# Kernel tuning notes

Measured on AMD Instinct MI355X. Metric: run time of the kernel, lower is better.

## Reference

```python
import jax, jax.numpy as jnp
import numpy as np

B, K, D = 2, 2048, 1024
H, DQ, DV = 16, 64, 64
DFF = 4096
ATT_SIZE = 256
LN_EPS = 1e-5


def _layernorm(x, g, b):
    mu = jnp.mean(x, axis=-1, keepdims=True)
    var = jnp.mean(jnp.square(x - mu), axis=-1, keepdims=True)
    return (x - mu) * jax.lax.rsqrt(var + LN_EPS) * g + b


def setup_inputs() -> dict:
    key = jax.random.key(0)
    ks = jax.random.split(key, 16)
    s = lambda d: 1.0 / np.sqrt(d)
    return {
        "x": jax.random.normal(ks[0], (B, K, D), dtype=jnp.float32),
        "Wq": jax.random.normal(ks[1], (D, H * DQ), dtype=jnp.float32) * s(D),
        "bq": jnp.zeros((H * DQ,), dtype=jnp.float32),
        "Wk": jax.random.normal(ks[2], (D, H * DQ), dtype=jnp.float32) * s(D),
        "bk": jnp.zeros((H * DQ,), dtype=jnp.float32),
        "Wv": jax.random.normal(ks[3], (D, H * DV), dtype=jnp.float32) * s(D),
        "bv": jnp.zeros((H * DV,), dtype=jnp.float32),
        "Wo": jax.random.normal(ks[4], (H * DV, D), dtype=jnp.float32) * s(H * DV),
        "bo": jnp.zeros((D,), dtype=jnp.float32),
        "W1": jax.random.normal(ks[5], (D, DFF), dtype=jnp.float32) * s(D),
        "b1": jnp.zeros((DFF,), dtype=jnp.float32),
        "W2": jax.random.normal(ks[6], (DFF, D), dtype=jnp.float32) * s(DFF),
        "b2": jnp.zeros((D,), dtype=jnp.float32),
        "ln1_g": jnp.ones((D,), dtype=jnp.float32),
        "ln1_b": jnp.zeros((D,), dtype=jnp.float32),
        "ln2_g": jnp.ones((D,), dtype=jnp.float32),
        "ln2_b": jnp.zeros((D,), dtype=jnp.float32),
    }


def reference(x, Wq, bq, Wk, bk, Wv, bv, Wo, bo, W1, b1, W2, b2,
              ln1_g, ln1_b, ln2_g, ln2_b):
    b, k, d = x.shape
    # --- multi-head attention (heads formed by chunking last dim) ---
    q = (x @ Wq + bq).reshape(b, k, H, DQ)  # [b,k,h,dq]
    kk = (x @ Wk + bk).reshape(b, k, H, DQ)
    v = (x @ Wv + bv).reshape(b, k, H, DV)
    # NOTE: original scales by sqrt(K) (sequence length), not sqrt(d_q)
    scores = jnp.einsum('bshd,bthd->bhst', q, kk) / jnp.sqrt(jnp.float32(k))
    idx = jnp.arange(k)
    band_mask = jnp.abs(idx[:, None] - idx[None, :]) > ATT_SIZE  # [k,k] bool
    scores = jnp.where(band_mask[None, None], -jnp.inf, scores)
    attn = jax.nn.softmax(scores, axis=-1)
    ctx = jnp.einsum('bhst,bthd->bshd', attn, v).reshape(b, k, H * DV)
    sa = ctx @ Wo + bo
    x1 = _layernorm(sa + x, ln1_g, ln1_b)
    # --- position-wise FFN (exact GELU as torch F.gelu default) ---
    ff = (jax.nn.gelu(x1 @ W1 + b1, approximate=False)) @ W2 + b2
    return _layernorm(ff + x1, ln2_g, ln2_b)
```

## Files before the change

kernel.cpp:

```cpp
#include <hip/hip_runtime.h>
#include <cstdint>
#include <math.h>

typedef unsigned short u16;
typedef __attribute__((ext_vector_type(8))) short bf16x8;
typedef __attribute__((ext_vector_type(4))) float f32x4;

#define DEVI __device__ __forceinline__

DEVI u16 f2bf(float f) {
  union { float f; uint32_t u; } v; v.f = f;
  return (u16)((v.u + 0x7FFFu + ((v.u >> 16) & 1u)) >> 16);
}
DEVI float bf2f(u16 h) {
  union { uint32_t u; float f; } v; v.u = ((uint32_t)h) << 16;
  return v.f;
}

DEVI void gload16(const void* g, void* l) {
  __builtin_amdgcn_global_load_lds(
      (const __attribute__((address_space(1))) void*)g,
      (__attribute__((address_space(3))) void*)l, 16, 0, 0);
}

DEVI float gelu_fast(float u) {
  float u2 = u * u;
  float t = __builtin_fmaf(0.044715f * u2, u, u);
  float e = __expf(1.5957691216057308f * t);
  float r = __builtin_amdgcn_rcpf(1.0f + e);
  return u - u * r;
}

DEVI void tcvt_body(const float* __restrict__ W, u16* __restrict__ Wt,
                    int Kd, int N, int n0, int k0, float* t) {
  const int r = threadIdx.x >> 4, c4 = (threadIdx.x & 15) * 4;
#pragma unroll
  for (int p = 0; p < 4; ++p) {
    int row = p * 16 + r;
    float4 f = *(const float4*)(W + (size_t)(k0 + row) * N + n0 + c4);
    *(float4*)&t[row * 68 + c4] = f;
  }
  __syncthreads();
#pragma unroll
  for (int p = 0; p < 4; ++p) {
    int n = p * 16 + r;
    float v0 = t[(c4 + 0) * 68 + n];
    float v1 = t[(c4 + 1) * 68 + n];
    float v2 = t[(c4 + 2) * 68 + n];
    float v3 = t[(c4 + 3) * 68 + n];
    uint32_t lo = (uint32_t)f2bf(v0) | ((uint32_t)f2bf(v1) << 16);
    uint32_t hi = (uint32_t)f2bf(v2) | ((uint32_t)f2bf(v3) << 16);
    *(uint2*)(Wt + (size_t)(n0 + n) * Kd + k0 + c4) = make_uint2(lo, hi);
  }
}

__global__ __launch_bounds__(256)
void prep_kernel(const float* __restrict__ Wq, const float* __restrict__ Wk,
                 const float* __restrict__ Wv, const float* __restrict__ Wo,
                 const float* __restrict__ W1, const float* __restrict__ W2,
                 const float* __restrict__ x, const float* __restrict__ bq,
                 const float* __restrict__ bk, const float* __restrict__ bv,
                 u16* __restrict__ WqkvT, u16* __restrict__ WoT,
                 u16* __restrict__ W1T, u16* __restrict__ W2T,
                 u16* __restrict__ xb, float* __restrict__ bqkv)
{
  __shared__ float t[64 * 68];
  const int b = blockIdx.x;
  if (b < 1024) {
    int wsel = b >> 8, tt = b & 255;
    const float* W = (wsel == 0) ? Wq : (wsel == 1) ? Wk : (wsel == 2) ? Wv : Wo;
    u16* dst = (wsel == 3) ? WoT : WqkvT + (size_t)wsel * 1024 * 1024;
    tcvt_body(W, dst, 1024, 1024, (tt & 15) * 64, (tt >> 4) * 64, t);
  } else if (b < 2048) {
    int tt = b - 1024;
    tcvt_body(W1, W1T, 1024, 4096, (tt & 63) * 64, (tt >> 6) * 64, t);
  } else if (b < 3072) {
    int tt = b - 2048;
    tcvt_body(W2, W2T, 4096, 1024, (tt & 15) * 64, (tt >> 4) * 64, t);
  } else if (b < 7168) {
    int i = ((b - 3072) * 256 + threadIdx.x) * 4;
    float4 f = *(const float4*)(x + i);
    uint32_t lo = (uint32_t)f2bf(f.x) | ((uint32_t)f2bf(f.y) << 16);
    uint32_t hi = (uint32_t)f2bf(f.z) | ((uint32_t)f2bf(f.w) << 16);
    *(uint2*)(xb + i) = make_uint2(lo, hi);
  } else {
    int i = (b - 7168) * 256 + threadIdx.x;
    const float* s = (i < 1024) ? bq : ((i < 2048) ? bk : bv);
    bqkv[i] = s[i & 1023];
  }
}

template<int MODE>
__global__ __launch_bounds__(256, 4)
void gemm_kernel(const u16* __restrict__ A, const u16* __restrict__ Bt,
                 const float* __restrict__ bias, void* __restrict__ C0,
                 void* __restrict__ C1, int N, int Kfull, int Kpart)
{
  __shared__ u16 As0[128 * 32], As1[128 * 32];
  __shared__ u16 Bs0[128 * 32], Bs1[128 * 32];
  const int tid = threadIdx.x;
  const int nbx = gridDim.x, nby = gridDim.y;
  int lin = blockIdx.y * nbx + blockIdx.x;
  int band = lin / (8 * nbx);
  int rem = lin - band * (8 * nbx);
  int gsz = min(nby - band * 8, 8);
  const int m0 = (band * 8 + rem % gsz) * 128;
  const int n0 = (rem / gsz) * 128;
  const int kbase = (MODE == 2) ? (int)blockIdx.z * Kpart : 0;
  const int w = tid >> 6, lane = tid & 63;
  const int wm = (w >> 1) * 64, wn = (w & 1) * 64;
  const int mr = lane & 15, ko = (lane >> 4) * 8;
  const int rq = (lane >> 4) * 4;
  const int w32 = w * 32;

  f32x4 acc[4][4];
#pragma unroll
  for (int i = 0; i < 4; ++i)
#pragma unroll
    for (int j = 0; j < 4; ++j) {
      f32x4 z = {0.f, 0.f, 0.f, 0.f};
      acc[i][j] = z;
    }

  const int lr = lane >> 2, lk = (lane & 3) * 8;
  const u16* aG = A  + (size_t)(m0 + w32 + lr) * Kfull + kbase + lk;
  const u16* bG = Bt + (size_t)(n0 + w32 + lr) * Kfull + kbase + lk;
  u16* aD00 = &As0[(w32 +  0) * 32];
  u16* aD01 = &As0[(w32 + 16) * 32];
  u16* aD10 = &As1[(w32 +  0) * 32];
  u16* aD11 = &As1[(w32 + 16) * 32];
  u16* bD00 = &Bs0[(w32 +  0) * 32];
  u16* bD01 = &Bs0[(w32 + 16) * 32];
  u16* bD10 = &Bs1[(w32 +  0) * 32];
  u16* bD11 = &Bs1[(w32 + 16) * 32];
  const size_t row16 = (size_t)16 * Kfull;

  for (int k0 = 0; k0 < Kpart; k0 += 64) {
    gload16(aG + k0,              aD00);
    gload16(aG + row16 + k0,      aD01);
    gload16(aG + k0 + 32,         aD10);
    gload16(aG + row16 + k0 + 32, aD11);
    gload16(bG + k0,              bD00);
    gload16(bG + row16 + k0,      bD01);
    gload16(bG + k0 + 32,         bD10);
    gload16(bG + row16 + k0 + 32, bD11);
    __syncthreads();
#pragma unroll
    for (int s = 0; s < 2; ++s) {
      const u16* Ap = s ? As1 : As0;
      const u16* Bp = s ? Bs1 : Bs0;
      bf16x8 af[4], bf[4];
#pragma unroll
      for (int i = 0; i < 4; ++i)
        af[i] = *(const bf16x8*)&Ap[(wm + i * 16 + mr) * 32 + ko];
#pragma unroll
      for (int j = 0; j < 4; ++j)
        bf[j] = *(const bf16x8*)&Bp[(wn + j * 16 + mr) * 32 + ko];
#pragma unroll
      for (int i = 0; i < 4; ++i)
#pragma unroll
        for (int j = 0; j < 4; ++j)
          acc[i][j] = __builtin_amdgcn_mfma_f32_16x16x32_bf16(bf[j], af[i], acc[i][j], 0, 0, 0);
    }
    __syncthreads();
  }

  if (MODE == 0) {
    if (n0 < 2048) {
#pragma unroll
      for (int i = 0; i < 4; ++i) {
        size_t mrow = (size_t)(m0 + wm + i * 16 + mr) * 2048;
#pragma unroll
        for (int j = 0; j < 4; ++j) {
          int nb = n0 + wn + j * 16 + rq;
          float4 b4 = *(const float4*)&bias[nb];
          uint32_t lo = (uint32_t)f2bf(acc[i][j][0] + b4.x) |
                        ((uint32_t)f2bf(acc[i][j][1] + b4.y) << 16);
          uint32_t hi = (uint32_t)f2bf(acc[i][j][2] + b4.z) |
                        ((uint32_t)f2bf(acc[i][j][3] + b4.w) << 16);
          *(uint2*)((u16*)C0 + mrow + nb) = make_uint2(lo, hi);
        }
      }
    } else {
#pragma unroll
      for (int i = 0; i < 4; ++i) {
        int mg = m0 + wm + i * 16 + mr;
#pragma unroll
        for (int j = 0; j < 4; ++j) {
          int nb = n0 + wn + j * 16 + rq;
          float4 b4 = *(const float4*)&bias[nb];
          int d = nb - 2048;
          ((u16*)C1)[(size_t)(d + 0) * 4096 + mg] = f2bf(acc[i][j][0] + b4.x);
          ((u16*)C1)[(size_t)(d + 1) * 4096 + mg] = f2bf(acc[i][j][1] + b4.y);
          ((u16*)C1)[(size_t)(d + 2) * 4096 + mg] = f2bf(acc[i][j][2] + b4.z);
          ((u16*)C1)[(size_t)(d + 3) * 4096 + mg] = f2bf(acc[i][j][3] + b4.w);
        }
      }
    }
  } else {
    const bool part1 = (MODE == 2) && (blockIdx.z == 1);
#pragma unroll
    for (int i = 0; i < 4; ++i) {
      size_t mrow = (size_t)(m0 + wm + i * 16 + mr) * N;
#pragma unroll
      for (int j = 0; j < 4; ++j) {
        int nb = n0 + wn + j * 16 + rq;
        if (MODE == 1) {
          float4 b4 = *(const float4*)&bias[nb];
          float v0 = gelu_fast(acc[i][j][0] + b4.x);
          float v1 = gelu_fast(acc[i][j][1] + b4.y);
          float v2 = gelu_fast(acc[i][j][2] + b4.z);
          float v3 = gelu_fast(acc[i][j][3] + b4.w);
          uint32_t lo = (uint32_t)f2bf(v0) | ((uint32_t)f2bf(v1) << 16);
          uint32_t hi = (uint32_t)f2bf(v2) | ((uint32_t)f2bf(v3) << 16);
          *(uint2*)((u16*)C0 + mrow + nb) = make_uint2(lo, hi);
        } else if (part1) {
          uint32_t lo = (uint32_t)f2bf(acc[i][j][0]) | ((uint32_t)f2bf(acc[i][j][1]) << 16);
          uint32_t hi = (uint32_t)f2bf(acc[i][j][2]) | ((uint32_t)f2bf(acc[i][j][3]) << 16);
          *(uint2*)((u16*)C1 + mrow + nb) = make_uint2(lo, hi);
        } else {
          float4 b4 = *(const float4*)&bias[nb];
          float4 ov;
          ov.x = acc[i][j][0] + b4.x;
          ov.y = acc[i][j][1] + b4.y;
          ov.z = acc[i][j][2] + b4.z;
          ov.w = acc[i][j][3] + b4.w;
          *(float4*)((float*)C0 + mrow + nb) = ov;
        }
      }
    }
  }
}

__global__ __launch_bounds__(256)
void attn_kernel(const u16* __restrict__ QKb, const u16* __restrict__ Vt,
                 u16* __restrict__ ctx)
{
  const int KS = 2048, HD = 1024;
  __shared__ u16 Qs[64 * 80];
  __shared__ u16 Ks[64 * 80];
  __shared__ u16 Vts[64 * 72];
  __shared__ u16 Ps[64 * 72];

  const int qt = blockIdx.x, hh = blockIdx.y, bb = blockIdx.z;
  const int s0 = qt * 64;
  const int tid = threadIdx.x, w = tid >> 6, lane = tid & 63;
  const int mr = lane & 15, ko = (lane >> 4) * 8, rq = (lane >> 4) * 4;
  const int sr = tid >> 3, sc = (tid & 7) * 8;
  const int vrow = tid >> 2, vtc = (tid & 3) * 16;
  const float qsc = 0.022097086912079608f;
  const int qg = s0 + w * 16 + mr;

#pragma unroll
  for (int p = 0; p < 2; ++p) {
    int row = p * 32 + sr;
    uint4 u = *(const uint4*)(QKb + (size_t)(bb * KS + s0 + row) * 2048 + hh * 64 + sc);
    *(uint4*)&Qs[row * 80 + sc] = u;
  }

  f32x4 accO[4];
#pragma unroll
  for (int j = 0; j < 4; ++j) { f32x4 z = {0.f,0.f,0.f,0.f}; accO[j] = z; }
  float lsum = 0.f;

  for (int c = 0; c < 9; ++c) {
    int tb = s0 - 256 + c * 64;
    if (tb < 0 || tb >= KS) continue;
    __syncthreads();
#pragma unroll
    for (int p = 0; p < 2; ++p) {
      int row = p * 32 + sr;
      uint4 uk = *(const uint4*)(QKb + (size_t)(bb * KS + tb + row) * 2048 + 1024 + hh * 64 + sc);
      *(uint4*)&Ks[row * 80 + sc] = uk;
    }
    {
      const u16* vsrc = Vt + (size_t)(hh * 64 + vrow) * 4096 + bb * KS + tb + vtc;
      *(uint4*)&Vts[vrow * 72 + vtc]     = *(const uint4*)vsrc;
      *(uint4*)&Vts[vrow * 72 + vtc + 8] = *(const uint4*)(vsrc + 8);
    }
    __syncthreads();

    f32x4 sacc[4];
#pragma unroll
    for (int j = 0; j < 4; ++j) { f32x4 z = {0.f,0.f,0.f,0.f}; sacc[j] = z; }
#pragma unroll
    for (int s = 0; s < 2; ++s) {
      bf16x8 aq = *(const bf16x8*)&Qs[(w * 16 + mr) * 80 + s * 32 + ko];
#pragma unroll
      for (int j = 0; j < 4; ++j) {
        bf16x8 bk = *(const bf16x8*)&Ks[(j * 16 + mr) * 80 + s * 32 + ko];
        sacc[j] = __builtin_amdgcn_mfma_f32_16x16x32_bf16(bk, aq, sacc[j], 0, 0, 0);
      }
    }

#pragma unroll
    for (int j = 0; j < 4; ++j) {
      int tgb = tb + j * 16 + rq;
      float p0, p1, p2, p3;
      {
        int d0 = qg - tgb;
        float s_ = sacc[j][0] * qsc;
        p0 = (d0 > 256 || d0 < -256) ? 0.f : __expf(s_);
        int d1 = d0 - 1; s_ = sacc[j][1] * qsc;
        p1 = (d1 > 256 || d1 < -256) ? 0.f : __expf(s_);
        int d2 = d0 - 2; s_ = sacc[j][2] * qsc;
        p2 = (d2 > 256 || d2 < -256) ? 0.f : __expf(s_);
        int d3 = d0 - 3; s_ = sacc[j][3] * qsc;
        p3 = (d3 > 256 || d3 < -256) ? 0.f : __expf(s_);
      }
      lsum += p0 + p1 + p2 + p3;
      uint32_t lo = (uint32_t)f2bf(p0) | ((uint32_t)f2bf(p1) << 16);
      uint32_t hi = (uint32_t)f2bf(p2) | ((uint32_t)f2bf(p3) << 16);
      *(uint2*)&Ps[(w * 16 + mr) * 72 + j * 16 + rq] = make_uint2(lo, hi);
    }
#pragma unroll
    for (int s = 0; s < 2; ++s) {
      bf16x8 ap = *(const bf16x8*)&Ps[(w * 16 + mr) * 72 + s * 32 + ko];
#pragma unroll
      for (int j = 0; j < 4; ++j) {
        bf16x8 bv = *(const bf16x8*)&Vts[(j * 16 + mr) * 72 + s * 32 + ko];
        accO[j] = __builtin_amdgcn_mfma_f32_16x16x32_bf16(bv, ap, accO[j], 0, 0, 0);
      }
    }
  }

  float l = lsum;
  l += __shfl_xor(l, 16, 64);
  l += __shfl_xor(l, 32, 64);
  float inv = 1.f / l;
  size_t base = (size_t)(bb * KS + qg) * HD + hh * 64;
#pragma unroll
  for (int j = 0; j < 4; ++j) {
    uint32_t lo = (uint32_t)f2bf(accO[j][0] * inv) | ((uint32_t)f2bf(accO[j][1] * inv) << 16);
    uint32_t hi = (uint32_t)f2bf(accO[j][2] * inv) | ((uint32_t)f2bf(accO[j][3] * inv) << 16);
    *(uint2*)(ctx + base + j * 16 + rq) = make_uint2(lo, hi);
  }
}

template<int V>
__global__ __launch_bounds__(256)
void ln_kernel(const float* __restrict__ a, const u16* __restrict__ ab,
               const void* __restrict__ res, const float* __restrict__ g,
               const float* __restrict__ be, void* __restrict__ out)
{
  __shared__ float red[8];
  const int row = blockIdx.x, tid = threadIdx.x;
  const int w = tid >> 6, lane = tid & 63;
  size_t base = (size_t)row * 1024 + tid * 4;
  float4 va = *(const float4*)(a + base);
  float v0 = va.x, v1 = va.y, v2 = va.z, v3 = va.w;
  {
    uint2 u = *(const uint2*)(ab + base);
    v0 += bf2f((u16)(u.x & 0xFFFFu));
    v1 += bf2f((u16)(u.x >> 16));
    v2 += bf2f((u16)(u.y & 0xFFFFu));
    v3 += bf2f((u16)(u.y >> 16));
  }
  if (V == 0) {
    float4 vb = *(const float4*)((const float*)res + base);
    v0 += vb.x; v1 += vb.y; v2 += vb.z; v3 += vb.w;
  } else {
    uint2 u = *(const uint2*)((const u16*)res + base);
    v0 += bf2f((u16)(u.x & 0xFFFFu));
    v1 += bf2f((u16)(u.x >> 16));
    v2 += bf2f((u16)(u.y & 0xFFFFu));
    v3 += bf2f((u16)(u.y >> 16));
  }
  float s1 = v0 + v1 + v2 + v3;
  float s2 = v0 * v0 + v1 * v1 + v2 * v2 + v3 * v3;
#pragma unroll
  for (int o = 32; o > 0; o >>= 1) {
    s1 += __shfl_xor(s1, o, 64);
    s2 += __shfl_xor(s2, o, 64);
  }
  if (lane == 0) { red[w] = s1; red[4 + w] = s2; }
  __syncthreads();
  s1 = red[0] + red[1] + red[2] + red[3];
  s2 = red[4] + red[5] + red[6] + red[7];
  float mu = s1 * (1.f / 1024.f);
  float var = s2 * (1.f / 1024.f) - mu * mu;
  float rs = rsqrtf(var + 1e-5f);
  float4 gv = *(const float4*)(g + tid * 4);
  float4 bv = *(const float4*)(be + tid * 4);
  float o0 = (v0 - mu) * rs * gv.x + bv.x;
  float o1 = (v1 - mu) * rs * gv.y + bv.y;
  float o2 = (v2 - mu) * rs * gv.z + bv.z;
  float o3 = (v3 - mu) * rs * gv.w + bv.w;
  if (V == 0) {
    uint32_t lo = (uint32_t)f2bf(o0) | ((uint32_t)f2bf(o1) << 16);
    uint32_t hi = (uint32_t)f2bf(o2) | ((uint32_t)f2bf(o3) << 16);
    *(uint2*)((u16*)out + base) = make_uint2(lo, hi);
  } else {
    float4 ov; ov.x = o0; ov.y = o1; ov.z = o2; ov.w = o3;
    *(float4*)((float*)out + base) = ov;
  }
}

extern "C" void kernel_launch(void* const* d_in, const int* in_sizes, int n_in,
                              void* d_out, int out_size, void* d_ws, size_t ws_size,
                              hipStream_t stream)
{
  (void)in_sizes; (void)n_in; (void)out_size; (void)ws_size;
  const float* x   = (const float*)d_in[0];
  const float* Wq  = (const float*)d_in[1];
  const float* bq  = (const float*)d_in[2];
  const float* Wk  = (const float*)d_in[3];
  const float* bk  = (const float*)d_in[4];
  const float* Wv  = (const float*)d_in[5];
  const float* bv  = (const float*)d_in[6];
  const float* Wo  = (const float*)d_in[7];
  const float* bo  = (const float*)d_in[8];
  const float* W1  = (const float*)d_in[9];
  const float* b1  = (const float*)d_in[10];
  const float* W2  = (const float*)d_in[11];
  const float* b2  = (const float*)d_in[12];
  const float* g1  = (const float*)d_in[13];
  const float* be1 = (const float*)d_in[14];
  const float* g2  = (const float*)d_in[15];
  const float* be2 = (const float*)d_in[16];

  char* ws = (char*)d_ws;
  const size_t MB = 1048576;
  u16*   W1T   = (u16*)(ws + 0 * MB);
  u16*   Y1    = (u16*)(ws + 0 * MB);
  u16*   xb    = (u16*)(ws + 8 * MB);
  u16*   X1b   = (u16*)(ws + 8 * MB);
  u16*   WqkvT = (u16*)(ws + 16 * MB);
  u16*   WoT   = (u16*)(ws + 22 * MB);
  u16*   QKb   = (u16*)(ws + 24 * MB);
  float* SA0   = (float*)(ws + 24 * MB);
  u16*   Hb    = (u16*)(ws + 24 * MB);
  u16*   Vt    = (u16*)(ws + 40 * MB);
  u16*   SA1   = (u16*)(ws + 40 * MB);
  float* bqkv  = (float*)(ws + 48 * MB);
  u16*   Cb    = (u16*)(ws + 48 * MB);
  u16*   W2T   = (u16*)(ws + 56 * MB);
  float* yout  = (float*)d_out;

  dim3 blk(256);
  prep_kernel<<<7180, blk, 0, stream>>>(Wq, Wk, Wv, Wo, W1, W2, x, bq, bk, bv,
                                        WqkvT, WoT, W1T, W2T, xb, bqkv);
  gemm_kernel<0><<<dim3(24, 32, 1), blk, 0, stream>>>(xb, WqkvT, bqkv, QKb, Vt, 3072, 1024, 1024);
  attn_kernel<<<dim3(32, 16, 2), blk, 0, stream>>>(QKb, Vt, Cb);
  gemm_kernel<2><<<dim3(8, 32, 2), blk, 0, stream>>>(Cb, WoT, bo, SA0, SA1, 1024, 1024, 512);
  ln_kernel<0><<<4096, blk, 0, stream>>>(SA0, SA1, x, g1, be1, X1b);
  gemm_kernel<1><<<dim3(32, 32, 1), blk, 0, stream>>>(X1b, W1T, b1, Hb, nullptr, 4096, 1024, 1024);
  gemm_kernel<2><<<dim3(8, 32, 2), blk, 0, stream>>>(Hb, W2T, b2, yout, Y1, 1024, 4096, 2048);
  ln_kernel<1><<<4096, blk, 0, stream>>>(yout, Y1, X1b, g2, be2, yout);
}
```

Baseline: 327.4 us.

## Store split-K partials in bf16, vectorize V-transpose stores via swapped MFMA operands

For the V columns of the QKV GEMM, the MFMA operands are swapped so each lane holds four consecutive rows, and the transposed V store becomes one 8-byte write instead of four scattered 2-byte writes. Both split-K partials of the Wo and W2 GEMMs are now stored as bf16 instead of one fp32 and one bf16. The layernorm kernels read three bf16 inputs, and the first LN uses the bf16 copy of x as its residual. This cuts global write and read traffic but adds bf16 rounding to the partial sums and the residual, which lowers accuracy.

Result: slower. 533.7 us (+63.0%).

```diff
diff --git a/kernel.cpp b/kernel.cpp
--- a/kernel.cpp
+++ b/kernel.cpp
@@ -112,6 +112,7 @@
   const int mr = lane & 15, ko = (lane >> 4) * 8;
   const int rq = (lane >> 4) * 4;
   const int w32 = w * 32;
+  const bool vblk = (MODE == 0) && (n0 >= 2048);
 
   f32x4 acc[4][4];
 #pragma unroll
@@ -156,17 +157,25 @@
 #pragma unroll
       for (int j = 0; j < 4; ++j)
         bf[j] = *(const bf16x8*)&Bp[(wn + j * 16 + mr) * 32 + ko];
-#pragma unroll
-      for (int i = 0; i < 4; ++i)
-#pragma unroll
-        for (int j = 0; j < 4; ++j)
-          acc[i][j] = __builtin_amdgcn_mfma_f32_16x16x32_bf16(bf[j], af[i], acc[i][j], 0, 0, 0);
+      if (!vblk) {
+#pragma unroll
+        for (int i = 0; i < 4; ++i)
+#pragma unroll
+          for (int j = 0; j < 4; ++j)
+            acc[i][j] = __builtin_amdgcn_mfma_f32_16x16x32_bf16(bf[j], af[i], acc[i][j], 0, 0, 0);
+      } else {
+#pragma unroll
+        for (int i = 0; i < 4; ++i)
+#pragma unroll
+          for (int j = 0; j < 4; ++j)
+            acc[i][j] = __builtin_amdgcn_mfma_f32_16x16x32_bf16(af[i], bf[j], acc[i][j], 0, 0, 0);
+      }
     }
     __syncthreads();
   }
 
   if (MODE == 0) {
-    if (n0 < 2048) {
+    if (!vblk) {
 #pragma unroll
       for (int i = 0; i < 4; ++i) {
         size_t mrow = (size_t)(m0 + wm + i * 16 + mr) * 2048;
@@ -184,16 +193,17 @@
     } else {
 #pragma unroll
       for (int i = 0; i < 4; ++i) {
-        int mg = m0 + wm + i * 16 + mr;
+        int mg = m0 + wm + i * 16 + rq;
 #pragma unroll
         for (int j = 0; j < 4; ++j) {
-          int nb = n0 + wn + j * 16 + rq;
-          float4 b4 = *(const float4*)&bias[nb];
-          int d = nb - 2048;
-          ((u16*)C1)[(size_t)(d + 0) * 4096 + mg] = f2bf(acc[i][j][0] + b4.x);
-          ((u16*)C1)[(size_t)(d + 1) * 4096 + mg] = f2bf(acc[i][j][1] + b4.y);
-          ((u16*)C1)[(size_t)(d + 2) * 4096 + mg] = f2bf(acc[i][j][2] + b4.z);
-          ((u16*)C1)[(size_t)(d + 3) * 4096 + mg] = f2bf(acc[i][j][3] + b4.w);
+          int ng = n0 + wn + j * 16 + mr;
+          float bv = bias[ng];
+          int d = ng - 2048;
+          uint32_t lo = (uint32_t)f2bf(acc[i][j][0] + bv) |
+                        ((uint32_t)f2bf(acc[i][j][1] + bv) << 16);
+          uint32_t hi = (uint32_t)f2bf(acc[i][j][2] + bv) |
+                        ((uint32_t)f2bf(acc[i][j][3] + bv) << 16);
+          *(uint2*)((u16*)C1 + (size_t)d * 4096 + mg) = make_uint2(lo, hi);
         }
       }
     }
@@ -205,28 +215,20 @@
 #pragma unroll
       for (int j = 0; j < 4; ++j) {
         int nb = n0 + wn + j * 16 + rq;
+        float v0 = acc[i][j][0], v1 = acc[i][j][1];
+        float v2 = acc[i][j][2], v3 = acc[i][j][3];
+        if (!part1) {
+          float4 b4 = *(const float4*)&bias[nb];
+          v0 += b4.x; v1 += b4.y; v2 += b4.z; v3 += b4.w;
+        }
         if (MODE == 1) {
-          float4 b4 = *(const float4*)&bias[nb];
-          float v0 = gelu_fast(acc[i][j][0] + b4.x);
-          float v1 = gelu_fast(acc[i][j][1] + b4.y);
-          float v2 = gelu_fast(acc[i][j][2] + b4.z);
-          float v3 = gelu_fast(acc[i][j][3] + b4.w);
-          uint32_t lo = (uint32_t)f2bf(v0) | ((uint32_t)f2bf(v1) << 16);
-          uint32_t hi = (uint32_t)f2bf(v2) | ((uint32_t)f2bf(v3) << 16);
-          *(uint2*)((u16*)C0 + mrow + nb) = make_uint2(lo, hi);
-        } else if (part1) {
-          uint32_t lo = (uint32_t)f2bf(acc[i][j][0]) | ((uint32_t)f2bf(acc[i][j][1]) << 16);
-          uint32_t hi = (uint32_t)f2bf(acc[i][j][2]) | ((uint32_t)f2bf(acc[i][j][3]) << 16);
-          *(uint2*)((u16*)C1 + mrow + nb) = make_uint2(lo, hi);
-        } else {
-          float4 b4 = *(const float4*)&bias[nb];
-          float4 ov;
-          ov.x = acc[i][j][0] + b4.x;
-          ov.y = acc[i][j][1] + b4.y;
-          ov.z = acc[i][j][2] + b4.z;
-          ov.w = acc[i][j][3] + b4.w;
-          *(float4*)((float*)C0 + mrow + nb) = ov;
+          v0 = gelu_fast(v0); v1 = gelu_fast(v1);
+          v2 = gelu_fast(v2); v3 = gelu_fast(v3);
         }
+        uint32_t lo = (uint32_t)f2bf(v0) | ((uint32_t)f2bf(v1) << 16);
+        uint32_t hi = (uint32_t)f2bf(v2) | ((uint32_t)f2bf(v3) << 16);
+        u16* dst = part1 ? (u16*)C1 : (u16*)C0;
+        *(uint2*)(dst + mrow + nb) = make_uint2(lo, hi);
       }
     }
   }
@@ -337,35 +339,28 @@
   }
 }
 
-template<int V>
+DEVI void bfadd4(const u16* p, size_t base, float& v0, float& v1, float& v2, float& v3) {
+  uint2 u = *(const uint2*)(p + base);
+  v0 += bf2f((u16)(u.x & 0xFFFFu));
+  v1 += bf2f((u16)(u.x >> 16));
+  v2 += bf2f((u16)(u.y & 0xFFFFu));
+  v3 += bf2f((u16)(u.y >> 16));
+}
+
+template<int OUT32>
 __global__ __launch_bounds__(256)
-void ln_kernel(const float* __restrict__ a, const u16* __restrict__ ab,
-               const void* __restrict__ res, const float* __restrict__ g,
+void ln_kernel(const u16* __restrict__ p0, const u16* __restrict__ p1,
+               const u16* __restrict__ res, const float* __restrict__ g,
                const float* __restrict__ be, void* __restrict__ out)
 {
   __shared__ float red[8];
   const int row = blockIdx.x, tid = threadIdx.x;
   const int w = tid >> 6, lane = tid & 63;
   size_t base = (size_t)row * 1024 + tid * 4;
-  float4 va = *(const float4*)(a + base);
-  float v0 = va.x, v1 = va.y, v2 = va.z, v3 = va.w;
-  {
-    uint2 u = *(const uint2*)(ab + base);
-    v0 += bf2f((u16)(u.x & 0xFFFFu));
-    v1 += bf2f((u16)(u.x >> 16));
-    v2 += bf2f((u16)(u.y & 0xFFFFu));
-    v3 += bf2f((u16)(u.y >> 16));
-  }
-  if (V == 0) {
-    float4 vb = *(const float4*)((const float*)res + base);
-    v0 += vb.x; v1 += vb.y; v2 += vb.z; v3 += vb.w;
-  } else {
-    uint2 u = *(const uint2*)((const u16*)res + base);
-    v0 += bf2f((u16)(u.x & 0xFFFFu));
-    v1 += bf2f((u16)(u.x >> 16));
-    v2 += bf2f((u16)(u.y & 0xFFFFu));
-    v3 += bf2f((u16)(u.y >> 16));
-  }
+  float v0 = 0.f, v1 = 0.f, v2 = 0.f, v3 = 0.f;
+  bfadd4(p0, base, v0, v1, v2, v3);
+  bfadd4(p1, base, v0, v1, v2, v3);
+  bfadd4(res, base, v0, v1, v2, v3);
   float s1 = v0 + v1 + v2 + v3;
   float s2 = v0 * v0 + v1 * v1 + v2 * v2 + v3 * v3;
 #pragma unroll
@@ -386,13 +381,13 @@
   float o1 = (v1 - mu) * rs * gv.y + bv.y;
   float o2 = (v2 - mu) * rs * gv.z + bv.z;
   float o3 = (v3 - mu) * rs * gv.w + bv.w;
-  if (V == 0) {
+  if (OUT32) {
+    float4 ov; ov.x = o0; ov.y = o1; ov.z = o2; ov.w = o3;
+    *(float4*)((float*)out + base) = ov;
+  } else {
     uint32_t lo = (uint32_t)f2bf(o0) | ((uint32_t)f2bf(o1) << 16);
     uint32_t hi = (uint32_t)f2bf(o2) | ((uint32_t)f2bf(o3) << 16);
     *(uint2*)((u16*)out + base) = make_uint2(lo, hi);
-  } else {
-    float4 ov; ov.x = o0; ov.y = o1; ov.z = o2; ov.w = o3;
-    *(float4*)((float*)out + base) = ov;
   }
 }
 
@@ -422,16 +417,17 @@
   char* ws = (char*)d_ws;
   const size_t MB = 1048576;
   u16*   W1T   = (u16*)(ws + 0 * MB);
-  u16*   Y1    = (u16*)(ws + 0 * MB);
+  u16*   Y0b   = (u16*)(ws + 0 * MB);
   u16*   xb    = (u16*)(ws + 8 * MB);
-  u16*   X1b   = (u16*)(ws + 8 * MB);
+  u16*   Y1b   = (u16*)(ws + 8 * MB);
   u16*   WqkvT = (u16*)(ws + 16 * MB);
+  u16*   X1b   = (u16*)(ws + 16 * MB);
   u16*   WoT   = (u16*)(ws + 22 * MB);
   u16*   QKb   = (u16*)(ws + 24 * MB);
-  float* SA0   = (float*)(ws + 24 * MB);
+  u16*   SA0b  = (u16*)(ws + 24 * MB);
+  u16*   SA1b  = (u16*)(ws + 32 * MB);
   u16*   Hb    = (u16*)(ws + 24 * MB);
   u16*   Vt    = (u16*)(ws + 40 * MB);
-  u16*   SA1   = (u16*)(ws + 40 * MB);
   float* bqkv  = (float*)(ws + 48 * MB);
   u16*   Cb    = (u16*)(ws + 48 * MB);
   u16*   W2T   = (u16*)(ws + 56 * MB);
@@ -442,9 +438,9 @@
                                         WqkvT, WoT, W1T, W2T, xb, bqkv);
   gemm_kernel<0><<<dim3(24, 32, 1), blk, 0, stream>>>(xb, WqkvT, bqkv, QKb, Vt, 3072, 1024, 1024);
   attn_kernel<<<dim3(32, 16, 2), blk, 0, stream>>>(QKb, Vt, Cb);
-  gemm_kernel<2><<<dim3(8, 32, 2), blk, 0, stream>>>(Cb, WoT, bo, SA0, SA1, 1024, 1024, 512);
-  ln_kernel<0><<<4096, blk, 0, stream>>>(SA0, SA1, x, g1, be1, X1b);
+  gemm_kernel<2><<<dim3(8, 32, 2), blk, 0, stream>>>(Cb, WoT, bo, SA0b, SA1b, 1024, 1024, 512);
+  ln_kernel<0><<<4096, blk, 0, stream>>>(SA0b, SA1b, xb, g1, be1, X1b);
   gemm_kernel<1><<<dim3(32, 32, 1), blk, 0, stream>>>(X1b, W1T, b1, Hb, nullptr, 4096, 1024, 1024);
-  gemm_kernel<2><<<dim3(8, 32, 2), blk, 0, stream>>>(Hb, W2T, b2, yout, Y1, 1024, 4096, 2048);
-  ln_kernel<1><<<4096, blk, 0, stream>>>(yout, Y1, X1b, g2, be2, yout);
-}
+  gemm_kernel<2><<<dim3(8, 32, 2), blk, 0, stream>>>(Hb, W2T, b2, Y0b, Y1b, 1024, 4096, 2048);
+  ln_kernel<1><<<4096, blk, 0, stream>>>(Y0b, Y1b, X1b, g2, be2, yout);
+}
```
